# Optimization experiments

Measured on AMD Instinct MI355X. Metric: run time of the kernel, lower is better.

Reference implementation:

```python
import jax, jax.numpy as jnp
from jax import lax
import numpy as np

B, T, V = 2048, 128, 25
H = 512          # num_hidden
NUM_CLASSES = 100


def setup_inputs() -> dict:
    key = jax.random.key(0)
    ks = jax.random.split(key, 7)
    messages = jax.random.normal(ks[0], (B, T, V), dtype=jnp.float32)
    # LSTMCell params (PyTorch layout: weight_ih [4H, V], weight_hh [4H, H], gate order i,f,g,o)
    W_ih = jax.random.normal(ks[1], (4 * H, V), dtype=jnp.float32) * (1.0 / np.sqrt(V))
    W_hh = jax.random.normal(ks[2], (4 * H, H), dtype=jnp.float32) * (1.0 / np.sqrt(H))
    b_ih = jnp.zeros((4 * H,), dtype=jnp.float32)
    # forget-gate bias initialized to 1 (as in initialize_parameters)
    b_hh = jnp.zeros((4 * H,), dtype=jnp.float32).at[H:2 * H].set(1.0)
    W_fc = jax.random.normal(ks[3], (NUM_CLASSES, H), dtype=jnp.float32) * (1.0 / np.sqrt(H))
    b_fc = jnp.zeros((NUM_CLASSES,), dtype=jnp.float32)
    return {"messages": messages, "W_ih": W_ih, "W_hh": W_hh,
            "b_ih": b_ih, "b_hh": b_hh, "W_fc": W_fc, "b_fc": b_fc}


def reference(messages, W_ih, W_hh, b_ih, b_hh, W_fc, b_fc):
    b, t, v = messages.shape
    h_dim = W_hh.shape[1]
    # Batch the input-to-hidden projection across all timesteps up front: [B,T,4H]
    x_proj = jnp.einsum('btv,gv->btg', messages, W_ih) + b_ih + b_hh
    xs = jnp.swapaxes(x_proj, 0, 1)  # [T, B, 4H] for scan over time

    def step(carry, x_g):
        h, c = carry
        gates = x_g + h @ W_hh.T                       # [B, 4H]
        i, f, g, o = jnp.split(gates, 4, axis=-1)      # PyTorch gate order i,f,g,o
        i = jax.nn.sigmoid(i)
        f = jax.nn.sigmoid(f)
        g = jnp.tanh(g)
        o = jax.nn.sigmoid(o)
        c = f * c + i * g
        h = o * jnp.tanh(c)
        return (h, c), None

    init = (jnp.zeros((b, h_dim), dtype=messages.dtype),
            jnp.zeros((b, h_dim), dtype=messages.dtype))
    (h_last, _), _ = lax.scan(step, init, xs)
    return h_last @ W_fc.T + b_fc  # [B, num_classes]
```

## Files before the change

kernel.cpp:

```cpp
#include <hip/hip_runtime.h>

#define BB 2048
#define TT 128
#define VV 25
#define HH 512
#define NC 100

typedef __attribute__((ext_vector_type(8))) _Float16 half8;
typedef __attribute__((ext_vector_type(4))) float f32x4;

__device__ __forceinline__ float fsigmoid(float x) { return 1.0f / (1.0f + __expf(-x)); }
__device__ __forceinline__ float ftanh(float x) {
    float e = __expf(2.0f * x);
    return 1.0f - 2.0f / (e + 1.0f);
}

__device__ __forceinline__ void bar_nodrain() {
    asm volatile("s_waitcnt lgkmcnt(0)" ::: "memory");
    __builtin_amdgcn_sched_barrier(0);
    __builtin_amdgcn_s_barrier();
    asm volatile("" ::: "memory");
}

__global__ __launch_bounds__(256) void prep_whh_t(const float* __restrict__ W,
                                                  _Float16* __restrict__ WT) {
    int i = blockIdx.x * 256 + threadIdx.x;
    int n = i & 2047, kq = i >> 11;
    half8 h8;
    #pragma unroll
    for (int j = 0; j < 8; ++j) h8[j] = (_Float16)W[(size_t)n * HH + kq * 8 + j];
    ((half8*)WT)[(size_t)kq * 2048 + n] = h8;
}

__global__ __launch_bounds__(256) void prep_wih_t(const float* __restrict__ W,
                                                  _Float16* __restrict__ WT) {
    int i = blockIdx.x * 256 + threadIdx.x;
    int n = i & 2047, kq4 = i >> 11;
    half8 h8;
    #pragma unroll
    for (int j = 0; j < 8; ++j) {
        int k = kq4 * 8 + j;
        h8[j] = (k < VV) ? (_Float16)W[(size_t)n * VV + k] : (_Float16)0.0f;
    }
    ((half8*)WT)[(size_t)(64 + kq4) * 2048 + n] = h8;
}

__global__ __launch_bounds__(256, 2) void lstm_step(
    const float* __restrict__ msg, int t,
    const _Float16* __restrict__ WT,
    const float* __restrict__ b_ih, const float* __restrict__ b_hh,
    const _Float16* __restrict__ hin, _Float16* __restrict__ hout,
    float* __restrict__ c)
{
    const int b0 = blockIdx.x * 64;
    const int j0 = blockIdx.y * 32;
    const int tid = threadIdx.x;
    const int lane = tid & 63;
    const int w = tid >> 6;
    const int wm = w & 1, wn = w >> 1;
    const int col = lane & 15, quad = lane >> 4;
    const int jj = j0 + wn * 16 + col;
    const bool first = (t == 0);

    __shared__ _Float16 Abuf[2][64][72];

    f32x4 acc[2][4];
    #pragma unroll
    for (int g = 0; g < 4; ++g) {
        float bias = b_ih[g * HH + jj] + b_hh[g * HH + jj];
        f32x4 bv = {bias, bias, bias, bias};
        acc[0][g] = bv;
        acc[1][g] = bv;
    }

    const int arow = tid >> 2, aseg = (tid & 3) << 4;
    const _Float16* aph = hin + (size_t)(b0 + arow) * HH + aseg;

    const half8* WT8 = (const half8*)WT;
    int bidx[4];
    #pragma unroll
    for (int g = 0; g < 4; ++g) bidx[g] = quad * 2048 + g * HH + jj;

    half8 Bs[4][4];
    half8 ra[2];
    float xv[2][8];

    if (!first) {
        ra[0] = *(const half8*)(aph);
        ra[1] = *(const half8*)(aph + 8);
        #pragma unroll
        for (int pc = 0; pc < 4; ++pc)
            #pragma unroll
            for (int g = 0; g < 4; ++g) Bs[pc][g] = WT8[pc * 8192 + bidx[g]];
        *(half8*)&Abuf[0][arow][aseg]     = ra[0];
        *(half8*)&Abuf[0][arow][aseg + 8] = ra[1];
        ra[0] = *(const half8*)(aph + 64);
        ra[1] = *(const half8*)(aph + 72);
        bar_nodrain();

        #pragma unroll
        for (int it = 0; it < 8; ++it) {
            const int buf = it & 1;
            #pragma unroll
            for (int kk = 0; kk < 2; ++kk) {
                const int cc = it * 2 + kk;
                const int sl = cc & 3;
                half8 ahf[2];
                #pragma unroll
                for (int tm = 0; tm < 2; ++tm)
                    ahf[tm] = *(const half8*)&Abuf[buf][wm * 32 + tm * 16 + col][kk * 32 + quad * 8];
                #pragma unroll
                for (int tm = 0; tm < 2; ++tm)
                    #pragma unroll
                    for (int g = 0; g < 4; ++g)
                        acc[tm][g] = __builtin_amdgcn_mfma_f32_16x16x32_f16(ahf[tm], Bs[sl][g], acc[tm][g], 0, 0, 0);
                const int pf = cc + 4;
                if (pf <= 16) {
                    #pragma unroll
                    for (int g = 0; g < 4; ++g) Bs[sl][g] = WT8[pf * 8192 + bidx[g]];
                }
            }
            if (it < 7) {
                *(half8*)&Abuf[buf ^ 1][arow][aseg]     = ra[0];
                *(half8*)&Abuf[buf ^ 1][arow][aseg + 8] = ra[1];
                if (it < 6) {
                    const int kt = (it + 2) * 64;
                    ra[0] = *(const half8*)(aph + kt);
                    ra[1] = *(const half8*)(aph + kt + 8);
                } else {
                    #pragma unroll
                    for (int tm = 0; tm < 2; ++tm) {
                        const size_t mb = ((size_t)(b0 + wm * 32 + tm * 16 + col) * TT + t) * VV;
                        #pragma unroll
                        for (int j = 0; j < 8; ++j) {
                            int k = quad * 8 + j;
                            xv[tm][j] = (k < VV) ? msg[mb + k] : 0.0f;
                        }
                    }
                }
                bar_nodrain();
            }
        }
    } else {
        #pragma unroll
        for (int tm = 0; tm < 2; ++tm) {
            const size_t mb = ((size_t)(b0 + wm * 32 + tm * 16 + col) * TT + t) * VV;
            #pragma unroll
            for (int j = 0; j < 8; ++j) {
                int k = quad * 8 + j;
                xv[tm][j] = (k < VV) ? msg[mb + k] : 0.0f;
            }
        }
        #pragma unroll
        for (int g = 0; g < 4; ++g) Bs[0][g] = WT8[16 * 8192 + bidx[g]];
    }

    float cv[2][4];
    if (!first) {
        #pragma unroll
        for (int tm = 0; tm < 2; ++tm)
            #pragma unroll
            for (int reg = 0; reg < 4; ++reg) {
                int b = b0 + wm * 32 + tm * 16 + quad * 4 + reg;
                cv[tm][reg] = c[(size_t)b * HH + jj];
            }
    }

    {
        half8 ahf[2];
        #pragma unroll
        for (int tm = 0; tm < 2; ++tm) {
            half8 xh;
            #pragma unroll
            for (int j = 0; j < 8; ++j) xh[j] = (_Float16)xv[tm][j];
            ahf[tm] = xh;
        }
        #pragma unroll
        for (int tm = 0; tm < 2; ++tm)
            #pragma unroll
            for (int g = 0; g < 4; ++g)
                acc[tm][g] = __builtin_amdgcn_mfma_f32_16x16x32_f16(ahf[tm], Bs[0][g], acc[tm][g], 0, 0, 0);
    }

    #pragma unroll
    for (int tm = 0; tm < 2; ++tm) {
        #pragma unroll
        for (int reg = 0; reg < 4; ++reg) {
            int b = b0 + wm * 32 + tm * 16 + quad * 4 + reg;
            size_t idx = (size_t)b * HH + jj;
            float i_ = fsigmoid(acc[tm][0][reg]);
            float f_ = fsigmoid(acc[tm][1][reg]);
            float g_ = ftanh(acc[tm][2][reg]);
            float o_ = fsigmoid(acc[tm][3][reg]);
            float cn = i_ * g_;
            if (!first) cn = __builtin_fmaf(f_, cv[tm][reg], cn);
            c[idx] = cn;
            hout[idx] = (_Float16)(o_ * ftanh(cn));
        }
    }
}

__global__ __launch_bounds__(256) void fc_kernel(
    const _Float16* __restrict__ h, const float* __restrict__ W_fc,
    const float* __restrict__ b_fc, float* __restrict__ out)
{
    __shared__ float hs[4][HH];
    const int b0 = blockIdx.x * 4;
    for (int i = threadIdx.x; i < 4 * HH; i += 256) {
        int r = i >> 9, k = i & 511;
        hs[r][k] = (float)h[(size_t)(b0 + r) * HH + k];
    }
    __syncthreads();
    const int tid = threadIdx.x;
    if (tid < 2 * NC) {
        int r = tid / NC, cls = tid % NC;
        const float4* wv = (const float4*)(W_fc + (size_t)cls * HH);
        const float4* h0 = (const float4*)hs[r];
        const float4* h1 = (const float4*)hs[r + 2];
        float s0 = 0.0f, s1 = 0.0f;
        #pragma unroll 4
        for (int k = 0; k < HH / 4; ++k) {
            float4 ww = wv[k];
            float4 a0 = h0[k], a1 = h1[k];
            s0 += a0.x * ww.x + a0.y * ww.y + a0.z * ww.z + a0.w * ww.w;
            s1 += a1.x * ww.x + a1.y * ww.y + a1.z * ww.z + a1.w * ww.w;
        }
        out[(size_t)(b0 + r) * NC + cls] = s0 + b_fc[cls];
        out[(size_t)(b0 + r + 2) * NC + cls] = s1 + b_fc[cls];
    }
}

extern "C" void kernel_launch(void* const* d_in, const int* in_sizes, int n_in,
                              void* d_out, int out_size, void* d_ws, size_t ws_size,
                              hipStream_t stream) {
    const float* msg  = (const float*)d_in[0];
    const float* W_ih = (const float*)d_in[1];
    const float* W_hh = (const float*)d_in[2];
    const float* b_ih = (const float*)d_in[3];
    const float* b_hh = (const float*)d_in[4];
    const float* W_fc = (const float*)d_in[5];
    const float* b_fc = (const float*)d_in[6];
    float* out = (float*)d_out;

    float*    c  = (float*)d_ws;
    _Float16* h0 = (_Float16*)(c + (size_t)BB * HH);
    _Float16* h1 = h0 + (size_t)BB * HH;
    _Float16* WT = h1 + (size_t)BB * HH;

    prep_whh_t<<<512, 256, 0, stream>>>(W_hh, WT);
    prep_wih_t<<<32, 256, 0, stream>>>(W_ih, WT);

    _Float16 *hin = h0, *hout = h1;
    for (int t = 0; t < TT; ++t) {
        lstm_step<<<dim3(BB / 64, HH / 32), 256, 0, stream>>>(
            msg, t, WT, b_ih, b_hh, hin, hout, c);
        _Float16* tmp = hin; hin = hout; hout = tmp;
    }
    fc_kernel<<<BB / 4, 256, 0, stream>>>(hin, W_fc, b_fc, out);
}
```

Before: 1.650 ms.

## Replace per-timestep launches with persistent LSTM kernel using per-group spin barriers

```diff
diff --git a/kernel.cpp b/kernel.cpp
--- a/kernel.cpp
+++ b/kernel.cpp
@@ -15,7 +15,23 @@
     return 1.0f - 2.0f / (e + 1.0f);
 }
 
-__device__ __forceinline__ void bar_nodrain() {
+__device__ __forceinline__ half8 gload_c(const _Float16* p) {
+    half8 r;
+    asm volatile("global_load_dwordx4 %0, %1, off sc0 sc1" : "=v"(r) : "v"(p) : "memory");
+    return r;
+}
+__device__ __forceinline__ void gstore_c(_Float16* p, _Float16 v) {
+    asm volatile("global_store_short %0, %1, off sc0 sc1" :: "v"(p), "v"(v) : "memory");
+}
+__device__ __forceinline__ void wait_vm0() {
+    asm volatile("s_waitcnt vmcnt(0)" ::: "memory");
+    __builtin_amdgcn_sched_barrier(0);
+}
+__device__ __forceinline__ void wait_vm8() {
+    asm volatile("s_waitcnt vmcnt(8)" ::: "memory");
+    __builtin_amdgcn_sched_barrier(0);
+}
+__device__ __forceinline__ void bar_lgkm() {
     asm volatile("s_waitcnt lgkmcnt(0)" ::: "memory");
     __builtin_amdgcn_sched_barrier(0);
     __builtin_amdgcn_s_barrier();
@@ -45,157 +61,176 @@
     ((half8*)WT)[(size_t)(64 + kq4) * 2048 + n] = h8;
 }
 
-__global__ __launch_bounds__(256, 2) void lstm_step(
-    const float* __restrict__ msg, int t,
+__global__ __launch_bounds__(256, 2) void lstm_persist(
+    const float* __restrict__ msg,
     const _Float16* __restrict__ WT,
     const float* __restrict__ b_ih, const float* __restrict__ b_hh,
-    const _Float16* __restrict__ hin, _Float16* __restrict__ hout,
-    float* __restrict__ c)
+    _Float16* __restrict__ h0g, _Float16* __restrict__ h1g,
+    unsigned* __restrict__ ctr)
 {
-    const int b0 = blockIdx.x * 64;
-    const int j0 = blockIdx.y * 32;
+    const int bx = blockIdx.x;
+    const int grp = bx >> 4;
+    const int b0 = grp * 64;
+    const int j0 = (bx & 15) * 32;
     const int tid = threadIdx.x;
     const int lane = tid & 63;
     const int w = tid >> 6;
     const int wm = w & 1, wn = w >> 1;
     const int col = lane & 15, quad = lane >> 4;
     const int jj = j0 + wn * 16 + col;
-    const bool first = (t == 0);
 
     __shared__ _Float16 Abuf[2][64][72];
 
-    f32x4 acc[2][4];
-    #pragma unroll
-    for (int g = 0; g < 4; ++g) {
-        float bias = b_ih[g * HH + jj] + b_hh[g * HH + jj];
-        f32x4 bv = {bias, bias, bias, bias};
-        acc[0][g] = bv;
-        acc[1][g] = bv;
-    }
+    float bias[4];
+    #pragma unroll
+    for (int g = 0; g < 4; ++g) bias[g] = b_ih[g * HH + jj] + b_hh[g * HH + jj];
 
     const int arow = tid >> 2, aseg = (tid & 3) << 4;
-    const _Float16* aph = hin + (size_t)(b0 + arow) * HH + aseg;
+    const size_t aoff = (size_t)(b0 + arow) * HH + aseg;
+    const _Float16* a0 = h0g + aoff;
+    const _Float16* a1 = h1g + aoff;
 
     const half8* WT8 = (const half8*)WT;
     int bidx[4];
     #pragma unroll
     for (int g = 0; g < 4; ++g) bidx[g] = quad * 2048 + g * HH + jj;
 
-    half8 Bs[4][4];
-    half8 ra[2];
+    const size_t soff = (size_t)(b0 + wm * 32 + quad * 4) * HH + jj;
+    _Float16* s0 = h0g + soff;
+    _Float16* s1 = h1g + soff;
+
+    unsigned* cnt = ctr + grp * 16;
+
+    float cv[2][4] = {{0.f,0.f,0.f,0.f},{0.f,0.f,0.f,0.f}};
+
+    const float* mp[2];
+    #pragma unroll
+    for (int tm = 0; tm < 2; ++tm)
+        mp[tm] = msg + (size_t)(b0 + wm * 32 + tm * 16 + col) * TT * VV;
+
     float xv[2][8];
-
-    if (!first) {
-        ra[0] = *(const half8*)(aph);
-        ra[1] = *(const half8*)(aph + 8);
+    #pragma unroll
+    for (int tm = 0; tm < 2; ++tm)
         #pragma unroll
-        for (int pc = 0; pc < 4; ++pc)
-            #pragma unroll
-            for (int g = 0; g < 4; ++g) Bs[pc][g] = WT8[pc * 8192 + bidx[g]];
-        *(half8*)&Abuf[0][arow][aseg]     = ra[0];
-        *(half8*)&Abuf[0][arow][aseg + 8] = ra[1];
-        ra[0] = *(const half8*)(aph + 64);
-        ra[1] = *(const half8*)(aph + 72);
-        bar_nodrain();
-
+        for (int j = 0; j < 8; ++j) {
+            int k = quad * 8 + j;
+            xv[tm][j] = (k < VV) ? mp[tm][k] : 0.0f;
+        }
+
+    half8 Bs[2][4];
+    #pragma unroll
+    for (int g = 0; g < 4; ++g) Bs[0][g] = WT8[16 * 8192 + bidx[g]];
+
+    for (int t = 0; t < TT; ++t) {
+        f32x4 acc[2][4];
         #pragma unroll
-        for (int it = 0; it < 8; ++it) {
-            const int buf = it & 1;
-            #pragma unroll
-            for (int kk = 0; kk < 2; ++kk) {
-                const int cc = it * 2 + kk;
-                const int sl = cc & 3;
-                half8 ahf[2];
-                #pragma unroll
-                for (int tm = 0; tm < 2; ++tm)
-                    ahf[tm] = *(const half8*)&Abuf[buf][wm * 32 + tm * 16 + col][kk * 32 + quad * 8];
-                #pragma unroll
-                for (int tm = 0; tm < 2; ++tm)
+        for (int g = 0; g < 4; ++g) {
+            f32x4 bv = {bias[g], bias[g], bias[g], bias[g]};
+            acc[0][g] = bv;
+            acc[1][g] = bv;
+        }
+
+        if (t > 0) {
+            const _Float16* aph = (t & 1) ? a1 : a0;
+
+            half8 ra0 = gload_c(aph);
+            half8 ra1 = gload_c(aph + 8);
+            wait_vm0();
+            *(half8*)&Abuf[0][arow][aseg]     = ra0;
+            *(half8*)&Abuf[0][arow][aseg + 8] = ra1;
+            ra0 = gload_c(aph + 64);
+            ra1 = gload_c(aph + 72);
+            bar_lgkm();
+
+            #pragma unroll
+            for (int it = 0; it < 8; ++it) {
+                const int buf = it & 1;
+                #pragma unroll
+                for (int kk = 0; kk < 2; ++kk) {
+                    const int cc = it * 2 + kk;
+                    const int sl = cc & 1;
+                    half8 ahf[2];
                     #pragma unroll
-                    for (int g = 0; g < 4; ++g)
-                        acc[tm][g] = __builtin_amdgcn_mfma_f32_16x16x32_f16(ahf[tm], Bs[sl][g], acc[tm][g], 0, 0, 0);
-                const int pf = cc + 4;
-                if (pf <= 16) {
+                    for (int tm = 0; tm < 2; ++tm)
+                        ahf[tm] = *(const half8*)&Abuf[buf][wm * 32 + tm * 16 + col][kk * 32 + quad * 8];
                     #pragma unroll
-                    for (int g = 0; g < 4; ++g) Bs[sl][g] = WT8[pf * 8192 + bidx[g]];
-                }
-            }
-            if (it < 7) {
-                *(half8*)&Abuf[buf ^ 1][arow][aseg]     = ra[0];
-                *(half8*)&Abuf[buf ^ 1][arow][aseg + 8] = ra[1];
-                if (it < 6) {
-                    const int kt = (it + 2) * 64;
-                    ra[0] = *(const half8*)(aph + kt);
-                    ra[1] = *(const half8*)(aph + kt + 8);
-                } else {
-                    #pragma unroll
-                    for (int tm = 0; tm < 2; ++tm) {
-                        const size_t mb = ((size_t)(b0 + wm * 32 + tm * 16 + col) * TT + t) * VV;
+                    for (int tm = 0; tm < 2; ++tm)
                         #pragma unroll
-                        for (int j = 0; j < 8; ++j) {
-                            int k = quad * 8 + j;
-                            xv[tm][j] = (k < VV) ? msg[mb + k] : 0.0f;
-                        }
+                        for (int g = 0; g < 4; ++g)
+                            acc[tm][g] = __builtin_amdgcn_mfma_f32_16x16x32_f16(ahf[tm], Bs[sl][g], acc[tm][g], 0, 0, 0);
+                    const int pf = cc + 2;
+                    if (pf <= 16) {
+                        #pragma unroll
+                        for (int g = 0; g < 4; ++g) Bs[sl][g] = WT8[pf * 8192 + bidx[g]];
                     }
                 }
-                bar_nodrain();
-            }
-        }
-    } else {
-        #pragma unroll
-        for (int tm = 0; tm < 2; ++tm) {
-            const size_t mb = ((size_t)(b0 + wm * 32 + tm * 16 + col) * TT + t) * VV;
-            #pragma unroll
-            for (int j = 0; j < 8; ++j) {
-                int k = quad * 8 + j;
-                xv[tm][j] = (k < VV) ? msg[mb + k] : 0.0f;
-            }
-        }
-        #pragma unroll
-        for (int g = 0; g < 4; ++g) Bs[0][g] = WT8[16 * 8192 + bidx[g]];
-    }
-
-    float cv[2][4];
-    if (!first) {
+                if (it < 7) {
+                    wait_vm8();
+                    *(half8*)&Abuf[buf ^ 1][arow][aseg]     = ra0;
+                    *(half8*)&Abuf[buf ^ 1][arow][aseg + 8] = ra1;
+                    if (it < 6) {
+                        ra0 = gload_c(aph + (it + 2) * 64);
+                        ra1 = gload_c(aph + (it + 2) * 64 + 8);
+                    }
+                    bar_lgkm();
+                }
+            }
+        }
+
+        {
+            half8 ahf[2];
+            #pragma unroll
+            for (int tm = 0; tm < 2; ++tm) {
+                half8 xh;
+                #pragma unroll
+                for (int j = 0; j < 8; ++j) xh[j] = (_Float16)xv[tm][j];
+                ahf[tm] = xh;
+            }
+            #pragma unroll
+            for (int tm = 0; tm < 2; ++tm)
+                #pragma unroll
+                for (int g = 0; g < 4; ++g)
+                    acc[tm][g] = __builtin_amdgcn_mfma_f32_16x16x32_f16(ahf[tm], Bs[0][g], acc[tm][g], 0, 0, 0);
+        }
+
+        _Float16* hop = (t & 1) ? s0 : s1;
         #pragma unroll
         for (int tm = 0; tm < 2; ++tm)
             #pragma unroll
             for (int reg = 0; reg < 4; ++reg) {
-                int b = b0 + wm * 32 + tm * 16 + quad * 4 + reg;
-                cv[tm][reg] = c[(size_t)b * HH + jj];
-            }
-    }
-
-    {
-        half8 ahf[2];
-        #pragma unroll
-        for (int tm = 0; tm < 2; ++tm) {
-            half8 xh;
-            #pragma unroll
-            for (int j = 0; j < 8; ++j) xh[j] = (_Float16)xv[tm][j];
-            ahf[tm] = xh;
-        }
-        #pragma unroll
-        for (int tm = 0; tm < 2; ++tm)
-            #pragma unroll
-            for (int g = 0; g < 4; ++g)
-                acc[tm][g] = __builtin_amdgcn_mfma_f32_16x16x32_f16(ahf[tm], Bs[0][g], acc[tm][g], 0, 0, 0);
-    }
-
-    #pragma unroll
-    for (int tm = 0; tm < 2; ++tm) {
-        #pragma unroll
-        for (int reg = 0; reg < 4; ++reg) {
-            int b = b0 + wm * 32 + tm * 16 + quad * 4 + reg;
-            size_t idx = (size_t)b * HH + jj;
-            float i_ = fsigmoid(acc[tm][0][reg]);
-            float f_ = fsigmoid(acc[tm][1][reg]);
-            float g_ = ftanh(acc[tm][2][reg]);
-            float o_ = fsigmoid(acc[tm][3][reg]);
-            float cn = i_ * g_;
-            if (!first) cn = __builtin_fmaf(f_, cv[tm][reg], cn);
-            c[idx] = cn;
-            hout[idx] = (_Float16)(o_ * ftanh(cn));
+                float i_ = fsigmoid(acc[tm][0][reg]);
+                float f_ = fsigmoid(acc[tm][1][reg]);
+                float g_ = ftanh(acc[tm][2][reg]);
+                float o_ = fsigmoid(acc[tm][3][reg]);
+                float cn = __builtin_fmaf(f_, cv[tm][reg], i_ * g_);
+                cv[tm][reg] = cn;
+                gstore_c(hop + (size_t)(tm * 16 + reg) * HH, (_Float16)(o_ * ftanh(cn)));
+            }
+
+        if (t + 1 < TT) {
+            #pragma unroll
+            for (int tm = 0; tm < 2; ++tm) mp[tm] += VV;
+            #pragma unroll
+            for (int tm = 0; tm < 2; ++tm)
+                #pragma unroll
+                for (int j = 0; j < 8; ++j) {
+                    int k = quad * 8 + j;
+                    xv[tm][j] = (k < VV) ? mp[tm][k] : 0.0f;
+                }
+            #pragma unroll
+            for (int g = 0; g < 4; ++g) {
+                Bs[0][g] = WT8[bidx[g]];
+                Bs[1][g] = WT8[8192 + bidx[g]];
+            }
+
+            __syncthreads();
+            if (tid == 0) {
+                __hip_atomic_fetch_add(cnt, 1u, __ATOMIC_RELEASE, __HIP_MEMORY_SCOPE_AGENT);
+                const unsigned tgt = 16u * (unsigned)(t + 1);
+                while (__hip_atomic_load(cnt, __ATOMIC_RELAXED, __HIP_MEMORY_SCOPE_AGENT) < tgt)
+                    __builtin_amdgcn_s_sleep(2);
+            }
+            __syncthreads();
         }
     }
 }
@@ -242,19 +277,17 @@
     const float* b_fc = (const float*)d_in[6];
     float* out = (float*)d_out;
 
-    float*    c  = (float*)d_ws;
-    _Float16* h0 = (_Float16*)(c + (size_t)BB * HH);
+    _Float16* h0 = (_Float16*)d_ws;
     _Float16* h1 = h0 + (size_t)BB * HH;
     _Float16* WT = h1 + (size_t)BB * HH;
+    unsigned* ctr = (unsigned*)(WT + (size_t)68 * 2048 * 8);
+
+    hipMemsetAsync(ctr, 0, 32 * 16 * sizeof(unsigned), stream);
 
     prep_whh_t<<<512, 256, 0, stream>>>(W_hh, WT);
     prep_wih_t<<<32, 256, 0, stream>>>(W_ih, WT);
 
-    _Float16 *hin = h0, *hout = h1;
-    for (int t = 0; t < TT; ++t) {
-        lstm_step<<<dim3(BB / 64, HH / 32), 256, 0, stream>>>(
-            msg, t, WT, b_ih, b_hh, hin, hout, c);
-        _Float16* tmp = hin; hin = hout; hout = tmp;
-    }
-    fc_kernel<<<BB / 4, 256, 0, stream>>>(hin, W_fc, b_fc, out);
-}
+    lstm_persist<<<512, 256, 0, stream>>>(msg, WT, b_ih, b_hh, h0, h1, ctr);
+
+    fc_kernel<<<BB / 4, 256, 0, stream>>>(h0, W_fc, b_fc, out);
+}
```

Result: slower. 3.242 ms (+96.5%).
